# Kernel tuning notes

Measured on AMD Instinct MI355X. Metric: run time of the kernel, lower is better.

## Reference

```python
import jax, jax.numpy as jnp
import numpy as np

M = 3          # num_modes
B = 64         # batch
D = 512        # feat_dim
HIST = 5       # history_len (deque pre-filled with HIST zero matrices)
SMOOTH = 0.8   # smooth_factor


def setup_inputs() -> dict:
    ks = jax.random.split(jax.random.key(0), 6)
    return {
        "x": jax.random.normal(ks[0], (M, B, D), jnp.float32),
        "proj_W": jax.random.normal(ks[1], (M, D, D), jnp.float32) * 0.02,
        "proj_b": jnp.zeros((M, D), jnp.float32),
        "ln_g": jnp.ones((M, D), jnp.float32),
        "ln_b": jnp.zeros((M, D), jnp.float32),
        "imp_W1": jax.random.normal(ks[2], (M, D // 4, D), jnp.float32) * 0.02,
        "imp_b1": jnp.zeros((M, D // 4), jnp.float32),
        "imp_W2": jax.random.normal(ks[3], (M, D, D // 4), jnp.float32) * 0.02,
        "imp_b2": jnp.zeros((M, D), jnp.float32),
        "gamma": jax.random.normal(ks[4], (M, M), jnp.float32) * 0.1,
        "modal_bias": jax.random.normal(ks[5], (M, M), jnp.float32) * 0.01,
        "constraint": jnp.ones((M,), jnp.float32) * 0.2,
    }


def _layernorm(v, g, b, eps=1e-5):
    mu = v.mean(-1, keepdims=True)
    var = ((v - mu) ** 2).mean(-1, keepdims=True)
    return (v - mu) / jnp.sqrt(var + eps) * g + b


def reference(x, proj_W, proj_b, ln_g, ln_b, imp_W1, imp_b1, imp_W2, imp_b2,
              gamma, modal_bias, constraint):
    scale = D ** 0.5
    # per-mode projector: Linear -> LayerNorm -> ReLU
    proj = [jax.nn.relu(_layernorm(x[i] @ proj_W[i].T + proj_b[i], ln_g[i], ln_b[i]))
            for i in range(M)]
    # channel importance: Linear -> ReLU -> Linear -> Sigmoid
    cw = [jax.nn.sigmoid(
              jax.nn.relu(proj[i] @ imp_W1[i].T + imp_b1[i]) @ imp_W2[i].T + imp_b2[i])
          for i in range(M)]
    wf = [proj[i] * cw[i] for i in range(M)]  # weighted features [B, D]

    interactions, scores = [], []
    for i in range(M):
        # deque holds HIST zero matrices; appends within this forward replace
        # zeros, so the running mean is sum(appended)/HIST.
        hist_sum = jnp.zeros((D, D), x.dtype)
        hist = hist_sum / HIST
        c = constraint[i]
        feats, gs = [], []
        for j in range(M):
            if i == j:
                continue
            cur = jnp.einsum('bd,be->bde', wf[i], wf[j]) / scale  # [B, D, D]
            constrained = hist + jnp.clip(cur - hist, -c, c)
            final = SMOOTH * constrained + (1.0 - SMOOTH) * cur
            # append detached batch-mean to history
            hist_sum = hist_sum + jax.lax.stop_gradient(final.mean(0))
            hist = hist_sum / HIST
            attn = jax.nn.softmax(final, axis=-1) + modal_bias[i, j]
            g = jax.nn.sigmoid(gamma[i, j])
            attended = jnp.einsum('bde,be->bd', attn, wf[j])  # bmm(attn, value)
            feats.append(g * attended + wf[i])
            gs.append(g)
        interactions.append(jnp.stack(feats).mean(0))
        scores.append(jnp.stack(gs).mean())
    fused = jnp.stack(interactions).mean(0)              # [B, D]
    attention_weights = jax.nn.softmax(jnp.stack(scores))  # [M]
    return fused, attention_weights
```

## Files before the change

kernel.cpp:

```cpp
#include <hip/hip_runtime.h>
#include <math.h>

#define M_ 3
#define B_ 64
#define D_ 512
#define H4 128
#define HIST_ 5
#define BD (B_ * D_)
#define INVSCALE 0.04419417382415922f
#define LOG2E 1.4426950408889634f

__device__ __forceinline__ float wave_sum64(float v) {
#pragma unroll
    for (int o = 32; o >= 1; o >>= 1) v += __shfl_xor(v, o, 64);
    return v;
}

__device__ __forceinline__ float sigmoidf(float x) {
    return 1.0f / (1.0f + __expf(-x));
}

__global__ __launch_bounds__(256) void k_proj(
    const float* __restrict__ x, const float* __restrict__ pW,
    const float* __restrict__ gamma, float* __restrict__ ypart,
    float* __restrict__ out)
{
    const int m    = blockIdx.x >> 8;
    const int r    = blockIdx.x & 255;
    const int kq   = r >> 6;
    const int rem2 = r & 63;
    const int dh   = rem2 >> 5;
    const int bp   = rem2 & 31;
    const int b0   = bp << 1;
    const int t    = threadIdx.x;
    const int d    = (dh << 8) + t;

    if (blockIdx.x < 128)
        out[(blockIdx.x << 8) + t] = 0.f;

    __shared__ __align__(16) float4 xs[2][32];
    if (t < 64) {
        const int rr = t >> 5, cc = t & 31;
        xs[rr][cc] = ((const float4*)(x + (size_t)(m * B_ + b0 + rr) * D_ + kq * 128))[cc];
    }
    __syncthreads();

    const float4* wr = (const float4*)(pW + (size_t)m * D_ * D_ + (size_t)d * D_ + kq * 128);
    float acc0 = 0.f, acc1 = 0.f;
#pragma unroll
    for (int k = 0; k < 32; ++k) {
        const float4 w = wr[k];
        const float4 a = xs[0][k];
        const float4 b = xs[1][k];
        acc0 = fmaf(w.x, a.x, acc0); acc0 = fmaf(w.y, a.y, acc0);
        acc0 = fmaf(w.z, a.z, acc0); acc0 = fmaf(w.w, a.w, acc0);
        acc1 = fmaf(w.x, b.x, acc1); acc1 = fmaf(w.y, b.y, acc1);
        acc1 = fmaf(w.z, b.z, acc1); acc1 = fmaf(w.w, b.w, acc1);
    }
    const size_t idx0 = (size_t)(m * B_ + b0) * 2048 + kq * 512 + d;
    ypart[idx0]        = acc0;
    ypart[idx0 + 2048] = acc1;

    if (blockIdx.x == 0 && t == 0) {
        const float g01 = sigmoidf(gamma[1]), g02 = sigmoidf(gamma[2]);
        const float g10 = sigmoidf(gamma[3]), g12 = sigmoidf(gamma[5]);
        const float g20 = sigmoidf(gamma[6]), g21 = sigmoidf(gamma[7]);
        const float s0 = 0.5f * (g01 + g02);
        const float s1 = 0.5f * (g10 + g12);
        const float s2 = 0.5f * (g20 + g21);
        const float mx = fmaxf(s0, fmaxf(s1, s2));
        const float e0 = __expf(s0 - mx), e1 = __expf(s1 - mx), e2 = __expf(s2 - mx);
        const float den = e0 + e1 + e2;
        out[BD + 0] = e0 / den;
        out[BD + 1] = e1 / den;
        out[BD + 2] = e2 / den;
    }
}

__global__ __launch_bounds__(512) void k_lnmlp(
    const float* __restrict__ ypart, const float* __restrict__ pb,
    const float* __restrict__ lg, const float* __restrict__ lb,
    const float* __restrict__ W1, const float* __restrict__ b1,
    const float* __restrict__ W2, const float* __restrict__ b2,
    float* __restrict__ wf, float* __restrict__ Ssum,
    float* __restrict__ out)
{
    const int m = blockIdx.x >> 6;
    const int b = blockIdx.x & 63;
    const int t = threadIdx.x;
    __shared__ __align__(16) float ps[D_];
    __shared__ __align__(16) float hs[H4];
    __shared__ __align__(16) float hpart[512];
    __shared__ float red[8];

    const size_t rbase = (size_t)(m * B_ + b) * 2048;
    const float y = ypart[rbase + t] + ypart[rbase + 512 + t]
                  + ypart[rbase + 1024 + t] + ypart[rbase + 1536 + t]
                  + pb[m * D_ + t];

    float s = wave_sum64(y);
    if ((t & 63) == 0) red[t >> 6] = s;
    __syncthreads();
    const float mean = (red[0]+red[1]+red[2]+red[3]+red[4]+red[5]+red[6]+red[7]) * (1.f / D_);
    __syncthreads();
    const float v = y - mean;
    float vs = wave_sum64(v * v);
    if ((t & 63) == 0) red[t >> 6] = vs;
    __syncthreads();
    const float inv = rsqrtf((red[0]+red[1]+red[2]+red[3]+red[4]+red[5]+red[6]+red[7]) * (1.f / D_) + 1e-5f);
    const float p = fmaxf(fmaf(v * inv, lg[m * D_ + t], lb[m * D_ + t]), 0.f);
    ps[t] = p;
    __syncthreads();

    {
        const int r = t & 127, seg = t >> 7;
        const float4* w1 = (const float4*)(W1 + ((size_t)m * H4 + r) * D_) + (seg << 5);
        const float4* pv = (const float4*)ps + (seg << 5);
        float a1 = 0.f;
#pragma unroll
        for (int k = 0; k < 32; ++k) {
            const float4 w = w1[k], pp = pv[k];
            a1 = fmaf(w.x, pp.x, a1); a1 = fmaf(w.y, pp.y, a1);
            a1 = fmaf(w.z, pp.z, a1); a1 = fmaf(w.w, pp.w, a1);
        }
        hpart[t] = a1;
    }
    __syncthreads();
    if (t < H4)
        hs[t] = fmaxf(hpart[t] + hpart[t + 128] + hpart[t + 256] + hpart[t + 384]
                      + b1[m * H4 + t], 0.f);
    __syncthreads();

    const float4* w2 = (const float4*)(W2 + ((size_t)m * D_ + t) * H4);
    const float4* hv = (const float4*)hs;
    float a2 = 0.f;
#pragma unroll
    for (int k = 0; k < H4 / 4; ++k) {
        const float4 w = w2[k], hh = hv[k];
        a2 = fmaf(w.x, hh.x, a2); a2 = fmaf(w.y, hh.y, a2);
        a2 = fmaf(w.z, hh.z, a2); a2 = fmaf(w.w, hh.w, a2);
    }
    const float cw = sigmoidf(a2 + b2[m * D_ + t]);
    const float wv = p * cw;
    wf[(size_t)(m * B_ + b) * D_ + t] = wv;
    atomicAdd(&out[b * D_ + t], wv * (1.f / 3.f));

    float tot = wave_sum64(wv);
    if ((t & 63) == 0) red[t >> 6] = tot;
    __syncthreads();
    if (t == 0)
        Ssum[m * B_ + b] = red[0]+red[1]+red[2]+red[3]+red[4]+red[5]+red[6]+red[7];
}

__global__ __launch_bounds__(256) void k_fuseAH(
    const float* __restrict__ wf, const float* __restrict__ constraint,
    const float* __restrict__ gamma, const float* __restrict__ mbias,
    const float* __restrict__ Ssum, float* __restrict__ HT,
    float* __restrict__ out)
{
    const int t = threadIdx.x;

    if (blockIdx.x < 768) {
        const int i    = blockIdx.x >> 8;
        const int rem  = blockIdx.x & 255;
        const int b0   = (rem >> 4) << 2;
        const int dc   = rem & 15;
        const int ln   = t & 31;
        const int d    = (dc << 5) + ln;
        const int esec = t >> 5;
        const int jA   = (i == 0) ? 1 : 0;

        const float c08 = constraint[i] * (0.8f * LOG2E);
        float a08[4], a02[4];
        const float* uAp[4];
#pragma unroll
        for (int bb = 0; bb < 4; ++bb) {
            const float a = wf[(size_t)i * BD + (b0 + bb) * D_ + d];
            a08[bb] = a * (0.8f * INVSCALE * LOG2E);
            a02[bb] = a * (0.2f * INVSCALE * LOG2E);
            uAp[bb] = wf + (size_t)jA * BD + (b0 + bb) * D_ + (esec << 6);
        }

        float sA[4] = {0.f, 0.f, 0.f, 0.f};
        float dA[4] = {0.f, 0.f, 0.f, 0.f};
#pragma unroll 2
        for (int e = 0; e < 64; e += 4) {
#pragma unroll
            for (int bb = 0; bb < 4; ++bb) {
                const float4 u4 = *(const float4*)(uAp[bb] + e);
                const float uu[4] = {u4.x, u4.y, u4.z, u4.w};
#pragma unroll
                for (int k = 0; k < 4; ++k) {
                    const float v1 = a08[bb] * uu[k];
                    const float v2 = fminf(v1, c08);
                    const float f  = fmaf(a02[bb], uu[k], v2);
                    const float p  = __builtin_amdgcn_exp2f(f);
                    sA[bb] += p;
                    dA[bb] = fmaf(p, uu[k], dA[bb]);
                }
            }
        }

        __shared__ __align__(8) float2 part[4][256];
#pragma unroll
        for (int bb = 0; bb < 4; ++bb)
            part[bb][t] = make_float2(sA[bb], dA[bb]);
        __syncthreads();
        if (t < 128) {
            const int bb = t >> 5;
            const int l  = t & 31;
            float Ss = 0.f, Sd = 0.f;
#pragma unroll
            for (int k = 0; k < 8; ++k) {
                const float2 pp = part[bb][l + (k << 5)];
                Ss += pp.x; Sd += pp.y;
            }
            const float gA = sigmoidf(gamma[i * 3 + jA]);
            const float pv = gA * (Sd / Ss + mbias[i * 3 + jA] * Ssum[jA * B_ + b0 + bb]);
            atomicAdd(&out[(b0 + bb) * D_ + (dc << 5) + l], pv * (1.f / 6.f));
        }
        return;
    }

    const int hb = blockIdx.x - 768;
    const int i  = hb >> 7;
    const int e0 = (hb & 127) << 2;
    const int j  = (i == 0) ? 1 : 0;
    const float c = constraint[i];
    const float* wfi = wf + (size_t)i * BD;
    const float* wfj = wf + (size_t)j * BD;

    float h0[4] = {0.f, 0.f, 0.f, 0.f};
    float h1[4] = {0.f, 0.f, 0.f, 0.f};
#pragma unroll 2
    for (int b = 0; b < B_; ++b) {
        const float a0 = wfi[b * D_ + t]       * INVSCALE;
        const float a1 = wfi[b * D_ + t + 256] * INVSCALE;
        const float4 u4 = *(const float4*)(wfj + b * D_ + e0);
        const float uu[4] = {u4.x, u4.y, u4.z, u4.w};
#pragma unroll
        for (int k = 0; k < 4; ++k) {
            float tt = a0 * uu[k]; float mm = fminf(tt, c);
            h0[k] = fmaf(0.8f, mm, fmaf(0.2f, tt, h0[k]));
            tt = a1 * uu[k]; mm = fminf(tt, c);
            h1[k] = fmaf(0.8f, mm, fmaf(0.2f, tt, h1[k]));
        }
    }
    const float hsc = LOG2E / (float)(B_ * HIST_);
    float* r0 = HT + ((size_t)(i << 9) + e0) * D_;
#pragma unroll
    for (int k = 0; k < 4; ++k) {
        r0[(size_t)k * D_ + t]       = h0[k] * hsc;
        r0[(size_t)k * D_ + t + 256] = h1[k] * hsc;
    }
}

__global__ __launch_bounds__(256) void k_passB(
    const float* __restrict__ wf, const float* __restrict__ constraint,
    const float* __restrict__ gamma, const float* __restrict__ mbias,
    const float* __restrict__ HT, const float* __restrict__ Ssum,
    float* __restrict__ out)
{
    const int i    = blockIdx.x >> 8;
    const int rem  = blockIdx.x & 255;
    const int b0   = (rem >> 4) << 2;
    const int dc   = rem & 15;
    const int t    = threadIdx.x;
    const int ln   = t & 31;
    const int d    = (dc << 5) + ln;
    const int esec = t >> 5;
    const int jB   = (i == 2) ? 1 : 2;

    const float cl = constraint[i] * LOG2E;
    float a[4];
    const float* uBp[4];
#pragma unroll
    for (int bb = 0; bb < 4; ++bb) {
        a[bb]  = wf[(size_t)i * BD + (b0 + bb) * D_ + d] * (INVSCALE * LOG2E);
        uBp[bb] = wf + (size_t)jB * BD + (b0 + bb) * D_ + (esec << 6);
    }
    const float* hp = HT + ((size_t)(i << 9) + (esec << 6)) * D_ + d;

    float sB[4] = {0.f, 0.f, 0.f, 0.f};
    float dB[4] = {0.f, 0.f, 0.f, 0.f};
#pragma unroll 2
    for (int e = 0; e < 64; e += 4) {
        float hh[4];
#pragma unroll
        for (int k = 0; k < 4; ++k) hh[k] = hp[(size_t)(e + k) * D_];
#pragma unroll
        for (int bb = 0; bb < 4; ++bb) {
            const float4 u4 = *(const float4*)(uBp[bb] + e);
            const float uu[4] = {u4.x, u4.y, u4.z, u4.w};
#pragma unroll
            for (int k = 0; k < 4; ++k) {
                const float tt = a[bb] * uu[k];
                const float df = tt - hh[k];
                const float mm = fminf(fmaxf(df, -cl), cl);
                const float f  = fmaf(0.8f, hh[k] + mm, 0.2f * tt);
                const float p  = __builtin_amdgcn_exp2f(f);
                sB[bb] += p;
                dB[bb] = fmaf(p, uu[k], dB[bb]);
            }
        }
    }

    __shared__ __align__(8) float2 part[4][256];
#pragma unroll
    for (int bb = 0; bb < 4; ++bb)
        part[bb][t] = make_float2(sB[bb], dB[bb]);
    __syncthreads();
    if (t < 128) {
        const int bb = t >> 5;
        const int l  = t & 31;
        float Ss = 0.f, Sd = 0.f;
#pragma unroll
        for (int k = 0; k < 8; ++k) {
            const float2 pp = part[bb][l + (k << 5)];
            Ss += pp.x; Sd += pp.y;
        }
        const float gB = sigmoidf(gamma[i * 3 + jB]);
        const float pv = gB * (Sd / Ss + mbias[i * 3 + jB] * Ssum[jB * B_ + b0 + bb]);
        atomicAdd(&out[(b0 + bb) * D_ + (dc << 5) + l], pv * (1.f / 6.f));
    }
}

extern "C" void kernel_launch(void* const* d_in, const int* in_sizes, int n_in,
                              void* d_out, int out_size, void* d_ws, size_t ws_size,
                              hipStream_t stream) {
    const float* x    = (const float*)d_in[0];
    const float* pW   = (const float*)d_in[1];
    const float* pb   = (const float*)d_in[2];
    const float* lg   = (const float*)d_in[3];
    const float* lb   = (const float*)d_in[4];
    const float* W1   = (const float*)d_in[5];
    const float* b1   = (const float*)d_in[6];
    const float* W2   = (const float*)d_in[7];
    const float* b2   = (const float*)d_in[8];
    const float* gamma= (const float*)d_in[9];
    const float* mb   = (const float*)d_in[10];
    const float* cons = (const float*)d_in[11];
    float* out = (float*)d_out;

    float* ws    = (float*)d_ws;
    float* wf    = ws;
    float* Ssum  = ws + 98304;
    float* HT    = ws + 98496;
    float* ypart = ws + 884928;

    k_proj  <<<dim3(768),     dim3(256), 0, stream>>>(x, pW, gamma, ypart, out);
    k_lnmlp <<<dim3(M_ * B_), dim3(512), 0, stream>>>(ypart, pb, lg, lb, W1, b1, W2, b2, wf, Ssum, out);
    k_fuseAH<<<dim3(1152),    dim3(256), 0, stream>>>(wf, cons, gamma, mb, Ssum, HT, out);
    k_passB <<<dim3(768),     dim3(256), 0, stream>>>(wf, cons, gamma, mb, HT, Ssum, out);
}
```

Baseline: 153.5 us.

## Fuse four kernel launches into one cooperative persistent kernel with grid syncs

Replaces the four separate launches (projection, layernorm+MLP, pass A with history, pass B) with a single cooperative kernel of 512 blocks that loops over the work items and separates the stages with grid.sync(). It keeps the old multi-launch path as a fallback if the cooperative launch fails. The aim is to remove launch gaps and inter-kernel overhead between the stages. In exchange, the grid is capped at 512 blocks, so stages with 768 or 1152 work items run in multiple rounds. The layernorm stage now runs on only 192 blocks of 256 threads, where it previously used 512 threads per block, and grid barriers add their own cost.

```diff
diff --git a/kernel.cpp b/kernel.cpp
--- a/kernel.cpp
+++ b/kernel.cpp
@@ -1,5 +1,8 @@
 #include <hip/hip_runtime.h>
+#include <hip/hip_cooperative_groups.h>
 #include <math.h>
+
+namespace cg = cooperative_groups;
 
 #define M_ 3
 #define B_ 64
@@ -9,6 +12,7 @@
 #define BD (B_ * D_)
 #define INVSCALE 0.04419417382415922f
 #define LOG2E 1.4426950408889634f
+#define GRID 512
 
 __device__ __forceinline__ float wave_sum64(float v) {
 #pragma unroll
@@ -18,6 +22,317 @@
 
 __device__ __forceinline__ float sigmoidf(float x) {
     return 1.0f / (1.0f + __expf(-x));
+}
+
+__global__ __launch_bounds__(256, 2) void k_fused(
+    const float* __restrict__ x, const float* __restrict__ pW,
+    const float* __restrict__ pb, const float* __restrict__ lg,
+    const float* __restrict__ lb, const float* __restrict__ W1,
+    const float* __restrict__ b1, const float* __restrict__ W2,
+    const float* __restrict__ b2, const float* __restrict__ gamma,
+    const float* __restrict__ mbias, const float* __restrict__ cons,
+    float* __restrict__ wf, float* __restrict__ Ssum,
+    float* __restrict__ HT, float* __restrict__ ypart,
+    float* __restrict__ out)
+{
+    cg::grid_group grid = cg::this_grid();
+    const int t   = threadIdx.x;
+    const int bid = blockIdx.x;
+    __shared__ __align__(16) float smem[2176];
+
+    if (bid < 128)
+        out[(bid << 8) + t] = 0.f;
+
+    for (int w = bid; w < 768; w += GRID) {
+        const int m    = w >> 8;
+        const int r    = w & 255;
+        const int kq   = r >> 6;
+        const int rem2 = r & 63;
+        const int dh   = rem2 >> 5;
+        const int b0   = (rem2 & 31) << 1;
+        const int d    = (dh << 8) + t;
+
+        float4* xs = (float4*)smem;
+        if (t < 64)
+            xs[t] = ((const float4*)(x + (size_t)(m * B_ + b0 + (t >> 5)) * D_ + kq * 128))[t & 31];
+        __syncthreads();
+
+        const float4* wr = (const float4*)(pW + (size_t)m * D_ * D_ + (size_t)d * D_ + kq * 128);
+        float acc0 = 0.f, acc1 = 0.f;
+#pragma unroll
+        for (int k = 0; k < 32; ++k) {
+            const float4 wv4 = wr[k];
+            const float4 a = xs[k];
+            const float4 b = xs[32 + k];
+            acc0 = fmaf(wv4.x, a.x, acc0); acc0 = fmaf(wv4.y, a.y, acc0);
+            acc0 = fmaf(wv4.z, a.z, acc0); acc0 = fmaf(wv4.w, a.w, acc0);
+            acc1 = fmaf(wv4.x, b.x, acc1); acc1 = fmaf(wv4.y, b.y, acc1);
+            acc1 = fmaf(wv4.z, b.z, acc1); acc1 = fmaf(wv4.w, b.w, acc1);
+        }
+        const size_t idx0 = (size_t)(m * B_ + b0) * 2048 + kq * 512 + d;
+        ypart[idx0]        = acc0;
+        ypart[idx0 + 2048] = acc1;
+        __syncthreads();
+    }
+
+    if (bid == 0 && t == 0) {
+        const float g01 = sigmoidf(gamma[1]), g02 = sigmoidf(gamma[2]);
+        const float g10 = sigmoidf(gamma[3]), g12 = sigmoidf(gamma[5]);
+        const float g20 = sigmoidf(gamma[6]), g21 = sigmoidf(gamma[7]);
+        const float s0 = 0.5f * (g01 + g02);
+        const float s1 = 0.5f * (g10 + g12);
+        const float s2 = 0.5f * (g20 + g21);
+        const float mx = fmaxf(s0, fmaxf(s1, s2));
+        const float e0 = __expf(s0 - mx), e1 = __expf(s1 - mx), e2 = __expf(s2 - mx);
+        const float den = e0 + e1 + e2;
+        out[BD + 0] = e0 / den;
+        out[BD + 1] = e1 / den;
+        out[BD + 2] = e2 / den;
+    }
+
+    grid.sync();
+
+    if (bid < 192) {
+        const int m = bid >> 6;
+        const int b = bid & 63;
+        float* ps    = smem;
+        float* hpart = smem + 512;
+        float* hs    = smem + 768;
+        float* red   = smem + 896;
+
+        const size_t rbase = (size_t)(m * B_ + b) * 2048;
+        const float y0 = ypart[rbase + t]        + ypart[rbase + 512 + t]
+                       + ypart[rbase + 1024 + t] + ypart[rbase + 1536 + t]
+                       + pb[m * D_ + t];
+        const float y1 = ypart[rbase + t + 256]        + ypart[rbase + 512 + t + 256]
+                       + ypart[rbase + 1024 + t + 256] + ypart[rbase + 1536 + t + 256]
+                       + pb[m * D_ + t + 256];
+
+        float s = wave_sum64(y0 + y1);
+        if ((t & 63) == 0) red[t >> 6] = s;
+        __syncthreads();
+        const float mean = (red[0] + red[1] + red[2] + red[3]) * (1.f / D_);
+        __syncthreads();
+        const float v0 = y0 - mean, v1 = y1 - mean;
+        float vs = wave_sum64(v0 * v0 + v1 * v1);
+        if ((t & 63) == 0) red[t >> 6] = vs;
+        __syncthreads();
+        const float inv = rsqrtf((red[0] + red[1] + red[2] + red[3]) * (1.f / D_) + 1e-5f);
+        const float p0 = fmaxf(fmaf(v0 * inv, lg[m * D_ + t],       lb[m * D_ + t]),       0.f);
+        const float p1 = fmaxf(fmaf(v1 * inv, lg[m * D_ + t + 256], lb[m * D_ + t + 256]), 0.f);
+        ps[t]       = p0;
+        ps[t + 256] = p1;
+        __syncthreads();
+
+        {
+            const int r = t & 127, seg = t >> 7;
+            const float4* w1 = (const float4*)(W1 + ((size_t)m * H4 + r) * D_) + (seg << 6);
+            const float4* pv = (const float4*)ps + (seg << 6);
+            float a1 = 0.f;
+#pragma unroll
+            for (int k = 0; k < 64; ++k) {
+                const float4 wq = w1[k], pp = pv[k];
+                a1 = fmaf(wq.x, pp.x, a1); a1 = fmaf(wq.y, pp.y, a1);
+                a1 = fmaf(wq.z, pp.z, a1); a1 = fmaf(wq.w, pp.w, a1);
+            }
+            hpart[t] = a1;
+        }
+        __syncthreads();
+        if (t < H4)
+            hs[t] = fmaxf(hpart[t] + hpart[t + 128] + b1[m * H4 + t], 0.f);
+        __syncthreads();
+
+        const float4* w2a = (const float4*)(W2 + ((size_t)m * D_ + t) * H4);
+        const float4* w2b = (const float4*)(W2 + ((size_t)m * D_ + t + 256) * H4);
+        const float4* hv  = (const float4*)hs;
+        float a2_0 = 0.f, a2_1 = 0.f;
+#pragma unroll
+        for (int k = 0; k < H4 / 4; ++k) {
+            const float4 hh4 = hv[k];
+            const float4 wA = w2a[k], wB = w2b[k];
+            a2_0 = fmaf(wA.x, hh4.x, a2_0); a2_0 = fmaf(wA.y, hh4.y, a2_0);
+            a2_0 = fmaf(wA.z, hh4.z, a2_0); a2_0 = fmaf(wA.w, hh4.w, a2_0);
+            a2_1 = fmaf(wB.x, hh4.x, a2_1); a2_1 = fmaf(wB.y, hh4.y, a2_1);
+            a2_1 = fmaf(wB.z, hh4.z, a2_1); a2_1 = fmaf(wB.w, hh4.w, a2_1);
+        }
+        const float wv0 = p0 * sigmoidf(a2_0 + b2[m * D_ + t]);
+        const float wv1 = p1 * sigmoidf(a2_1 + b2[m * D_ + t + 256]);
+        wf[(size_t)(m * B_ + b) * D_ + t]       = wv0;
+        wf[(size_t)(m * B_ + b) * D_ + t + 256] = wv1;
+        atomicAdd(&out[b * D_ + t],       wv0 * (1.f / 3.f));
+        atomicAdd(&out[b * D_ + t + 256], wv1 * (1.f / 3.f));
+
+        float tot = wave_sum64(wv0 + wv1);
+        if ((t & 63) == 0) red[t >> 6] = tot;
+        __syncthreads();
+        if (t == 0)
+            Ssum[m * B_ + b] = red[0] + red[1] + red[2] + red[3];
+    }
+
+    grid.sync();
+
+    for (int w = bid; w < 1152; w += GRID) {
+        if (w < 768) {
+            const int i    = w >> 8;
+            const int rem  = w & 255;
+            const int b0   = (rem >> 4) << 2;
+            const int dc   = rem & 15;
+            const int ln   = t & 31;
+            const int d    = (dc << 5) + ln;
+            const int esec = t >> 5;
+            const int jA   = (i == 0) ? 1 : 0;
+
+            const float c08 = cons[i] * (0.8f * LOG2E);
+            float a08[4], a02[4];
+            const float* uAp[4];
+#pragma unroll
+            for (int bb = 0; bb < 4; ++bb) {
+                const float a = wf[(size_t)i * BD + (b0 + bb) * D_ + d];
+                a08[bb] = a * (0.8f * INVSCALE * LOG2E);
+                a02[bb] = a * (0.2f * INVSCALE * LOG2E);
+                uAp[bb] = wf + (size_t)jA * BD + (b0 + bb) * D_ + (esec << 6);
+            }
+
+            float sA[4] = {0.f, 0.f, 0.f, 0.f};
+            float dA[4] = {0.f, 0.f, 0.f, 0.f};
+#pragma unroll 2
+            for (int e = 0; e < 64; e += 4) {
+#pragma unroll
+                for (int bb = 0; bb < 4; ++bb) {
+                    const float4 u4 = *(const float4*)(uAp[bb] + e);
+                    const float uu[4] = {u4.x, u4.y, u4.z, u4.w};
+#pragma unroll
+                    for (int k = 0; k < 4; ++k) {
+                        const float v1 = a08[bb] * uu[k];
+                        const float v2 = fminf(v1, c08);
+                        const float f  = fmaf(a02[bb], uu[k], v2);
+                        const float p  = __builtin_amdgcn_exp2f(f);
+                        sA[bb] += p;
+                        dA[bb] = fmaf(p, uu[k], dA[bb]);
+                    }
+                }
+            }
+
+            float2* part = (float2*)smem;
+#pragma unroll
+            for (int bb = 0; bb < 4; ++bb)
+                part[bb * 256 + t] = make_float2(sA[bb], dA[bb]);
+            __syncthreads();
+            if (t < 128) {
+                const int bb = t >> 5;
+                const int l  = t & 31;
+                float Ss = 0.f, Sd = 0.f;
+#pragma unroll
+                for (int k = 0; k < 8; ++k) {
+                    const float2 pp = part[bb * 256 + l + (k << 5)];
+                    Ss += pp.x; Sd += pp.y;
+                }
+                const float gA = sigmoidf(gamma[i * 3 + jA]);
+                const float pv = gA * (Sd / Ss + mbias[i * 3 + jA] * Ssum[jA * B_ + b0 + bb]);
+                atomicAdd(&out[(b0 + bb) * D_ + (dc << 5) + l], pv * (1.f / 6.f));
+            }
+            __syncthreads();
+        } else {
+            const int hw = w - 768;
+            const int i  = hw >> 7;
+            const int e0 = (hw & 127) << 2;
+            const int j  = (i == 0) ? 1 : 0;
+            const float c = cons[i];
+            const float* wfi = wf + (size_t)i * BD;
+            const float* wfj = wf + (size_t)j * BD;
+
+            float h0[4] = {0.f, 0.f, 0.f, 0.f};
+            float h1[4] = {0.f, 0.f, 0.f, 0.f};
+#pragma unroll 2
+            for (int b = 0; b < B_; ++b) {
+                const float a0 = wfi[b * D_ + t]       * INVSCALE;
+                const float a1 = wfi[b * D_ + t + 256] * INVSCALE;
+                const float4 u4 = *(const float4*)(wfj + b * D_ + e0);
+                const float uu[4] = {u4.x, u4.y, u4.z, u4.w};
+#pragma unroll
+                for (int k = 0; k < 4; ++k) {
+                    float tt = a0 * uu[k]; float mm = fminf(tt, c);
+                    h0[k] = fmaf(0.8f, mm, fmaf(0.2f, tt, h0[k]));
+                    tt = a1 * uu[k]; mm = fminf(tt, c);
+                    h1[k] = fmaf(0.8f, mm, fmaf(0.2f, tt, h1[k]));
+                }
+            }
+            const float hsc = LOG2E / (float)(B_ * HIST_);
+            float* r0 = HT + ((size_t)(i << 9) + e0) * D_;
+#pragma unroll
+            for (int k = 0; k < 4; ++k) {
+                r0[(size_t)k * D_ + t]       = h0[k] * hsc;
+                r0[(size_t)k * D_ + t + 256] = h1[k] * hsc;
+            }
+        }
+    }
+
+    grid.sync();
+
+    for (int w = bid; w < 768; w += GRID) {
+        const int i    = w >> 8;
+        const int rem  = w & 255;
+        const int b0   = (rem >> 4) << 2;
+        const int dc   = rem & 15;
+        const int ln   = t & 31;
+        const int d    = (dc << 5) + ln;
+        const int esec = t >> 5;
+        const int jB   = (i == 2) ? 1 : 2;
+
+        const float cl = cons[i] * LOG2E;
+        float a[4];
+        const float* uBp[4];
+#pragma unroll
+        for (int bb = 0; bb < 4; ++bb) {
+            a[bb]   = wf[(size_t)i * BD + (b0 + bb) * D_ + d] * (INVSCALE * LOG2E);
+            uBp[bb] = wf + (size_t)jB * BD + (b0 + bb) * D_ + (esec << 6);
+        }
+        const float* hp = HT + ((size_t)(i << 9) + (esec << 6)) * D_ + d;
+
+        float sB[4] = {0.f, 0.f, 0.f, 0.f};
+        float dB[4] = {0.f, 0.f, 0.f, 0.f};
+#pragma unroll 2
+        for (int e = 0; e < 64; e += 4) {
+            float hh[4];
+#pragma unroll
+            for (int k = 0; k < 4; ++k) hh[k] = hp[(size_t)(e + k) * D_];
+#pragma unroll
+            for (int bb = 0; bb < 4; ++bb) {
+                const float4 u4 = *(const float4*)(uBp[bb] + e);
+                const float uu[4] = {u4.x, u4.y, u4.z, u4.w};
+#pragma unroll
+                for (int k = 0; k < 4; ++k) {
+                    const float tt = a[bb] * uu[k];
+                    const float df = tt - hh[k];
+                    const float mm = fminf(fmaxf(df, -cl), cl);
+                    const float f  = fmaf(0.8f, hh[k] + mm, 0.2f * tt);
+                    const float p  = __builtin_amdgcn_exp2f(f);
+                    sB[bb] += p;
+                    dB[bb] = fmaf(p, uu[k], dB[bb]);
+                }
+            }
+        }
+
+        float2* part = (float2*)smem;
+#pragma unroll
+        for (int bb = 0; bb < 4; ++bb)
+            part[bb * 256 + t] = make_float2(sB[bb], dB[bb]);
+        __syncthreads();
+        if (t < 128) {
+            const int bb = t >> 5;
+            const int l  = t & 31;
+            float Ss = 0.f, Sd = 0.f;
+#pragma unroll
+            for (int k = 0; k < 8; ++k) {
+                const float2 pp = part[bb * 256 + l + (k << 5)];
+                Ss += pp.x; Sd += pp.y;
+            }
+            const float gB = sigmoidf(gamma[i * 3 + jB]);
+            const float pv = gB * (Sd / Ss + mbias[i * 3 + jB] * Ssum[jB * B_ + b0 + bb]);
+            atomicAdd(&out[(b0 + bb) * D_ + (dc << 5) + l], pv * (1.f / 6.f));
+        }
+        __syncthreads();
+    }
 }
 
 __global__ __launch_bounds__(256) void k_proj(
@@ -348,8 +663,17 @@
     float* HT    = ws + 98496;
     float* ypart = ws + 884928;
 
-    k_proj  <<<dim3(768),     dim3(256), 0, stream>>>(x, pW, gamma, ypart, out);
-    k_lnmlp <<<dim3(M_ * B_), dim3(512), 0, stream>>>(ypart, pb, lg, lb, W1, b1, W2, b2, wf, Ssum, out);
-    k_fuseAH<<<dim3(1152),    dim3(256), 0, stream>>>(wf, cons, gamma, mb, Ssum, HT, out);
-    k_passB <<<dim3(768),     dim3(256), 0, stream>>>(wf, cons, gamma, mb, HT, Ssum, out);
-}
+    void* args[] = { (void*)&x, (void*)&pW, (void*)&pb, (void*)&lg, (void*)&lb,
+                     (void*)&W1, (void*)&b1, (void*)&W2, (void*)&b2, (void*)&gamma,
+                     (void*)&mb, (void*)&cons, (void*)&wf, (void*)&Ssum,
+                     (void*)&HT, (void*)&ypart, (void*)&out };
+    hipError_t err = hipLaunchCooperativeKernel(
+        reinterpret_cast<const void*>(k_fused), dim3(GRID), dim3(256),
+        (void**)args, 0, stream);
+    if (err != hipSuccess) {
+        k_proj  <<<dim3(768),     dim3(256), 0, stream>>>(x, pW, gamma, ypart, out);
+        k_lnmlp <<<dim3(M_ * B_), dim3(512), 0, stream>>>(ypart, pb, lg, lb, W1, b1, W2, b2, wf, Ssum, out);
+        k_fuseAH<<<dim3(1152),    dim3(256), 0, stream>>>(wf, cons, gamma, mb, Ssum, HT, out);
+        k_passB <<<dim3(768),     dim3(256), 0, stream>>>(wf, cons, gamma, mb, HT, Ssum, out);
+    }
+}
```

After: 368.2 us. 2.4x slower.

## Fuse projection with LN/MLP and merge both attention passes into one kernel

Applied to the files above, without the earlier changes.

The projection GEMV now runs inside the LayerNorm/MLP kernel with one block per (mode,batch) row, so the ypart partial buffer and its kernel launch are gone. The history kernel is split out on its own, and the pass-A and pass-B attention kernels are merged into one kernel that loops over all three modes for 2 batch rows per block. That kernel writes the output directly, with no atomics and no zero-init. The cost is less parallelism: the projection now uses 192 blocks each reading a full 512x512 weight slice, and the merged pass uses 512 blocks.

```diff
diff --git a/kernel.cpp b/kernel.cpp
--- a/kernel.cpp
+++ b/kernel.cpp
@@ -20,46 +20,95 @@
     return 1.0f / (1.0f + __expf(-x));
 }
 
-__global__ __launch_bounds__(256) void k_proj(
+__global__ __launch_bounds__(512) void k_projln(
     const float* __restrict__ x, const float* __restrict__ pW,
-    const float* __restrict__ gamma, float* __restrict__ ypart,
+    const float* __restrict__ pb, const float* __restrict__ lg,
+    const float* __restrict__ lb, const float* __restrict__ W1,
+    const float* __restrict__ b1, const float* __restrict__ W2,
+    const float* __restrict__ b2, const float* __restrict__ gamma,
+    float* __restrict__ wf, float* __restrict__ Ssum,
     float* __restrict__ out)
 {
-    const int m    = blockIdx.x >> 8;
-    const int r    = blockIdx.x & 255;
-    const int kq   = r >> 6;
-    const int rem2 = r & 63;
-    const int dh   = rem2 >> 5;
-    const int bp   = rem2 & 31;
-    const int b0   = bp << 1;
-    const int t    = threadIdx.x;
-    const int d    = (dh << 8) + t;
-
-    if (blockIdx.x < 128)
-        out[(blockIdx.x << 8) + t] = 0.f;
-
-    __shared__ __align__(16) float4 xs[2][32];
-    if (t < 64) {
-        const int rr = t >> 5, cc = t & 31;
-        xs[rr][cc] = ((const float4*)(x + (size_t)(m * B_ + b0 + rr) * D_ + kq * 128))[cc];
-    }
-    __syncthreads();
-
-    const float4* wr = (const float4*)(pW + (size_t)m * D_ * D_ + (size_t)d * D_ + kq * 128);
-    float acc0 = 0.f, acc1 = 0.f;
-#pragma unroll
-    for (int k = 0; k < 32; ++k) {
-        const float4 w = wr[k];
-        const float4 a = xs[0][k];
-        const float4 b = xs[1][k];
-        acc0 = fmaf(w.x, a.x, acc0); acc0 = fmaf(w.y, a.y, acc0);
-        acc0 = fmaf(w.z, a.z, acc0); acc0 = fmaf(w.w, a.w, acc0);
-        acc1 = fmaf(w.x, b.x, acc1); acc1 = fmaf(w.y, b.y, acc1);
-        acc1 = fmaf(w.z, b.z, acc1); acc1 = fmaf(w.w, b.w, acc1);
-    }
-    const size_t idx0 = (size_t)(m * B_ + b0) * 2048 + kq * 512 + d;
-    ypart[idx0]        = acc0;
-    ypart[idx0 + 2048] = acc1;
+    const int m = blockIdx.x >> 6;
+    const int b = blockIdx.x & 63;
+    const int t = threadIdx.x;
+    __shared__ __align__(16) float xs[D_];
+    __shared__ __align__(16) float ps[D_];
+    __shared__ __align__(16) float hpart[512];
+    __shared__ __align__(16) float hs[H4];
+    __shared__ float red[8];
+
+    xs[t] = x[(size_t)(m * B_ + b) * D_ + t];
+    __syncthreads();
+
+    const float4* wr = (const float4*)(pW + ((size_t)m * D_ + t) * D_);
+    const float4* xv = (const float4*)xs;
+    float q[4];
+#pragma unroll
+    for (int qq = 0; qq < 4; ++qq) {
+        float acc = 0.f;
+#pragma unroll
+        for (int k = 0; k < 32; ++k) {
+            const float4 w = wr[(qq << 5) + k];
+            const float4 a = xv[(qq << 5) + k];
+            acc = fmaf(w.x, a.x, acc); acc = fmaf(w.y, a.y, acc);
+            acc = fmaf(w.z, a.z, acc); acc = fmaf(w.w, a.w, acc);
+        }
+        q[qq] = acc;
+    }
+    const float y = q[0] + q[1] + q[2] + q[3] + pb[m * D_ + t];
+
+    float s = wave_sum64(y);
+    if ((t & 63) == 0) red[t >> 6] = s;
+    __syncthreads();
+    const float mean = (red[0]+red[1]+red[2]+red[3]+red[4]+red[5]+red[6]+red[7]) * (1.f / D_);
+    __syncthreads();
+    const float v = y - mean;
+    float vs = wave_sum64(v * v);
+    if ((t & 63) == 0) red[t >> 6] = vs;
+    __syncthreads();
+    const float inv = rsqrtf((red[0]+red[1]+red[2]+red[3]+red[4]+red[5]+red[6]+red[7]) * (1.f / D_) + 1e-5f);
+    const float p = fmaxf(fmaf(v * inv, lg[m * D_ + t], lb[m * D_ + t]), 0.f);
+    ps[t] = p;
+    __syncthreads();
+
+    {
+        const int r = t & 127, seg = t >> 7;
+        const float4* w1 = (const float4*)(W1 + ((size_t)m * H4 + r) * D_) + (seg << 5);
+        const float4* pv = (const float4*)ps + (seg << 5);
+        float a1 = 0.f;
+#pragma unroll
+        for (int k = 0; k < 32; ++k) {
+            const float4 w = w1[k], pp = pv[k];
+            a1 = fmaf(w.x, pp.x, a1); a1 = fmaf(w.y, pp.y, a1);
+            a1 = fmaf(w.z, pp.z, a1); a1 = fmaf(w.w, pp.w, a1);
+        }
+        hpart[t] = a1;
+    }
+    __syncthreads();
+    if (t < H4)
+        hs[t] = fmaxf(hpart[t] + hpart[t + 128] + hpart[t + 256] + hpart[t + 384]
+                      + b1[m * H4 + t], 0.f);
+    __syncthreads();
+
+    const float4* w2 = (const float4*)(W2 + ((size_t)m * D_ + t) * H4);
+    const float4* hv = (const float4*)hs;
+    float a2 = 0.f;
+#pragma unroll
+    for (int k = 0; k < H4 / 4; ++k) {
+        const float4 w = w2[k], hh = hv[k];
+        a2 = fmaf(w.x, hh.x, a2); a2 = fmaf(w.y, hh.y, a2);
+        a2 = fmaf(w.z, hh.z, a2); a2 = fmaf(w.w, hh.w, a2);
+    }
+    const float cw = sigmoidf(a2 + b2[m * D_ + t]);
+    const float wv = p * cw;
+    wf[(size_t)(m * B_ + b) * D_ + t] = wv;
+
+    float tot = wave_sum64(wv);
+    if ((t & 63) == 0) red[t >> 6] = tot;
+    __syncthreads();
+    if (t == 0)
+        Ssum[m * B_ + b] = red[0]+red[1]+red[2]+red[3]+red[4]+red[5]+red[6]+red[7];
 
     if (blockIdx.x == 0 && t == 0) {
         const float g01 = sigmoidf(gamma[1]), g02 = sigmoidf(gamma[2]);
@@ -77,156 +126,15 @@
     }
 }
 
-__global__ __launch_bounds__(512) void k_lnmlp(
-    const float* __restrict__ ypart, const float* __restrict__ pb,
-    const float* __restrict__ lg, const float* __restrict__ lb,
-    const float* __restrict__ W1, const float* __restrict__ b1,
-    const float* __restrict__ W2, const float* __restrict__ b2,
-    float* __restrict__ wf, float* __restrict__ Ssum,
-    float* __restrict__ out)
+__global__ __launch_bounds__(256) void k_hist(
+    const float* __restrict__ wf, const float* __restrict__ cons,
+    float* __restrict__ HT)
 {
-    const int m = blockIdx.x >> 6;
-    const int b = blockIdx.x & 63;
-    const int t = threadIdx.x;
-    __shared__ __align__(16) float ps[D_];
-    __shared__ __align__(16) float hs[H4];
-    __shared__ __align__(16) float hpart[512];
-    __shared__ float red[8];
-
-    const size_t rbase = (size_t)(m * B_ + b) * 2048;
-    const float y = ypart[rbase + t] + ypart[rbase + 512 + t]
-                  + ypart[rbase + 1024 + t] + ypart[rbase + 1536 + t]
-                  + pb[m * D_ + t];
-
-    float s = wave_sum64(y);
-    if ((t & 63) == 0) red[t >> 6] = s;
-    __syncthreads();
-    const float mean = (red[0]+red[1]+red[2]+red[3]+red[4]+red[5]+red[6]+red[7]) * (1.f / D_);
-    __syncthreads();
-    const float v = y - mean;
-    float vs = wave_sum64(v * v);
-    if ((t & 63) == 0) red[t >> 6] = vs;
-    __syncthreads();
-    const float inv = rsqrtf((red[0]+red[1]+red[2]+red[3]+red[4]+red[5]+red[6]+red[7]) * (1.f / D_) + 1e-5f);
-    const float p = fmaxf(fmaf(v * inv, lg[m * D_ + t], lb[m * D_ + t]), 0.f);
-    ps[t] = p;
-    __syncthreads();
-
-    {
-        const int r = t & 127, seg = t >> 7;
-        const float4* w1 = (const float4*)(W1 + ((size_t)m * H4 + r) * D_) + (seg << 5);
-        const float4* pv = (const float4*)ps + (seg << 5);
-        float a1 = 0.f;
-#pragma unroll
-        for (int k = 0; k < 32; ++k) {
-            const float4 w = w1[k], pp = pv[k];
-            a1 = fmaf(w.x, pp.x, a1); a1 = fmaf(w.y, pp.y, a1);
-            a1 = fmaf(w.z, pp.z, a1); a1 = fmaf(w.w, pp.w, a1);
-        }
-        hpart[t] = a1;
-    }
-    __syncthreads();
-    if (t < H4)
-        hs[t] = fmaxf(hpart[t] + hpart[t + 128] + hpart[t + 256] + hpart[t + 384]
-                      + b1[m * H4 + t], 0.f);
-    __syncthreads();
-
-    const float4* w2 = (const float4*)(W2 + ((size_t)m * D_ + t) * H4);
-    const float4* hv = (const float4*)hs;
-    float a2 = 0.f;
-#pragma unroll
-    for (int k = 0; k < H4 / 4; ++k) {
-        const float4 w = w2[k], hh = hv[k];
-        a2 = fmaf(w.x, hh.x, a2); a2 = fmaf(w.y, hh.y, a2);
-        a2 = fmaf(w.z, hh.z, a2); a2 = fmaf(w.w, hh.w, a2);
-    }
-    const float cw = sigmoidf(a2 + b2[m * D_ + t]);
-    const float wv = p * cw;
-    wf[(size_t)(m * B_ + b) * D_ + t] = wv;
-    atomicAdd(&out[b * D_ + t], wv * (1.f / 3.f));
-
-    float tot = wave_sum64(wv);
-    if ((t & 63) == 0) red[t >> 6] = tot;
-    __syncthreads();
-    if (t == 0)
-        Ssum[m * B_ + b] = red[0]+red[1]+red[2]+red[3]+red[4]+red[5]+red[6]+red[7];
-}
-
-__global__ __launch_bounds__(256) void k_fuseAH(
-    const float* __restrict__ wf, const float* __restrict__ constraint,
-    const float* __restrict__ gamma, const float* __restrict__ mbias,
-    const float* __restrict__ Ssum, float* __restrict__ HT,
-    float* __restrict__ out)
-{
-    const int t = threadIdx.x;
-
-    if (blockIdx.x < 768) {
-        const int i    = blockIdx.x >> 8;
-        const int rem  = blockIdx.x & 255;
-        const int b0   = (rem >> 4) << 2;
-        const int dc   = rem & 15;
-        const int ln   = t & 31;
-        const int d    = (dc << 5) + ln;
-        const int esec = t >> 5;
-        const int jA   = (i == 0) ? 1 : 0;
-
-        const float c08 = constraint[i] * (0.8f * LOG2E);
-        float a08[4], a02[4];
-        const float* uAp[4];
-#pragma unroll
-        for (int bb = 0; bb < 4; ++bb) {
-            const float a = wf[(size_t)i * BD + (b0 + bb) * D_ + d];
-            a08[bb] = a * (0.8f * INVSCALE * LOG2E);
-            a02[bb] = a * (0.2f * INVSCALE * LOG2E);
-            uAp[bb] = wf + (size_t)jA * BD + (b0 + bb) * D_ + (esec << 6);
-        }
-
-        float sA[4] = {0.f, 0.f, 0.f, 0.f};
-        float dA[4] = {0.f, 0.f, 0.f, 0.f};
-#pragma unroll 2
-        for (int e = 0; e < 64; e += 4) {
-#pragma unroll
-            for (int bb = 0; bb < 4; ++bb) {
-                const float4 u4 = *(const float4*)(uAp[bb] + e);
-                const float uu[4] = {u4.x, u4.y, u4.z, u4.w};
-#pragma unroll
-                for (int k = 0; k < 4; ++k) {
-                    const float v1 = a08[bb] * uu[k];
-                    const float v2 = fminf(v1, c08);
-                    const float f  = fmaf(a02[bb], uu[k], v2);
-                    const float p  = __builtin_amdgcn_exp2f(f);
-                    sA[bb] += p;
-                    dA[bb] = fmaf(p, uu[k], dA[bb]);
-                }
-            }
-        }
-
-        __shared__ __align__(8) float2 part[4][256];
-#pragma unroll
-        for (int bb = 0; bb < 4; ++bb)
-            part[bb][t] = make_float2(sA[bb], dA[bb]);
-        __syncthreads();
-        if (t < 128) {
-            const int bb = t >> 5;
-            const int l  = t & 31;
-            float Ss = 0.f, Sd = 0.f;
-#pragma unroll
-            for (int k = 0; k < 8; ++k) {
-                const float2 pp = part[bb][l + (k << 5)];
-                Ss += pp.x; Sd += pp.y;
-            }
-            const float gA = sigmoidf(gamma[i * 3 + jA]);
-            const float pv = gA * (Sd / Ss + mbias[i * 3 + jA] * Ssum[jA * B_ + b0 + bb]);
-            atomicAdd(&out[(b0 + bb) * D_ + (dc << 5) + l], pv * (1.f / 6.f));
-        }
-        return;
-    }
-
-    const int hb = blockIdx.x - 768;
-    const int i  = hb >> 7;
-    const int e0 = (hb & 127) << 2;
+    const int t  = threadIdx.x;
+    const int i  = blockIdx.x >> 7;
+    const int e0 = (blockIdx.x & 127) << 2;
     const int j  = (i == 0) ? 1 : 0;
-    const float c = constraint[i];
+    const float c = cons[i];
     const float* wfi = wf + (size_t)i * BD;
     const float* wfj = wf + (size_t)j * BD;
 
@@ -255,73 +163,104 @@
     }
 }
 
-__global__ __launch_bounds__(256) void k_passB(
-    const float* __restrict__ wf, const float* __restrict__ constraint,
+__global__ __launch_bounds__(256) void k_pass(
+    const float* __restrict__ wf, const float* __restrict__ cons,
     const float* __restrict__ gamma, const float* __restrict__ mbias,
     const float* __restrict__ HT, const float* __restrict__ Ssum,
     float* __restrict__ out)
 {
-    const int i    = blockIdx.x >> 8;
-    const int rem  = blockIdx.x & 255;
-    const int b0   = (rem >> 4) << 2;
-    const int dc   = rem & 15;
+    const int bg   = blockIdx.x >> 4;
+    const int dc   = blockIdx.x & 15;
+    const int b0   = bg << 1;
     const int t    = threadIdx.x;
     const int ln   = t & 31;
     const int d    = (dc << 5) + ln;
     const int esec = t >> 5;
-    const int jB   = (i == 2) ? 1 : 2;
-
-    const float cl = constraint[i] * LOG2E;
-    float a[4];
-    const float* uBp[4];
-#pragma unroll
-    for (int bb = 0; bb < 4; ++bb) {
-        a[bb]  = wf[(size_t)i * BD + (b0 + bb) * D_ + d] * (INVSCALE * LOG2E);
-        uBp[bb] = wf + (size_t)jB * BD + (b0 + bb) * D_ + (esec << 6);
-    }
-    const float* hp = HT + ((size_t)(i << 9) + (esec << 6)) * D_ + d;
-
-    float sB[4] = {0.f, 0.f, 0.f, 0.f};
-    float dB[4] = {0.f, 0.f, 0.f, 0.f};
+
+    __shared__ __align__(16) float4 part[2][256];
+    float oacc = 0.f;
+
+#pragma unroll
+    for (int i = 0; i < 3; ++i) {
+        const int jA = (i == 0) ? 1 : 0;
+        const int jB = (i == 2) ? 1 : 2;
+        const float c08 = cons[i] * (0.8f * LOG2E);
+        const float cl  = cons[i] * LOG2E;
+
+        float a08[2], a02[2], aB[2];
+        const float* uA[2];
+        const float* uB[2];
+#pragma unroll
+        for (int bb = 0; bb < 2; ++bb) {
+            const float a = wf[(size_t)i * BD + (b0 + bb) * D_ + d];
+            a08[bb] = a * (0.8f * INVSCALE * LOG2E);
+            a02[bb] = a * (0.2f * INVSCALE * LOG2E);
+            aB[bb]  = a * (INVSCALE * LOG2E);
+            uA[bb] = wf + (size_t)jA * BD + (b0 + bb) * D_ + (esec << 6);
+            uB[bb] = wf + (size_t)jB * BD + (b0 + bb) * D_ + (esec << 6);
+        }
+        const float* hp = HT + ((size_t)(i << 9) + (esec << 6)) * D_ + d;
+
+        float sA[2] = {0.f, 0.f}, dA[2] = {0.f, 0.f};
+        float sB[2] = {0.f, 0.f}, dB[2] = {0.f, 0.f};
 #pragma unroll 2
-    for (int e = 0; e < 64; e += 4) {
-        float hh[4];
-#pragma unroll
-        for (int k = 0; k < 4; ++k) hh[k] = hp[(size_t)(e + k) * D_];
-#pragma unroll
-        for (int bb = 0; bb < 4; ++bb) {
-            const float4 u4 = *(const float4*)(uBp[bb] + e);
-            const float uu[4] = {u4.x, u4.y, u4.z, u4.w};
-#pragma unroll
-            for (int k = 0; k < 4; ++k) {
-                const float tt = a[bb] * uu[k];
-                const float df = tt - hh[k];
-                const float mm = fminf(fmaxf(df, -cl), cl);
-                const float f  = fmaf(0.8f, hh[k] + mm, 0.2f * tt);
-                const float p  = __builtin_amdgcn_exp2f(f);
-                sB[bb] += p;
-                dB[bb] = fmaf(p, uu[k], dB[bb]);
+        for (int e = 0; e < 64; e += 4) {
+            float hh[4];
+#pragma unroll
+            for (int k = 0; k < 4; ++k) hh[k] = hp[(size_t)(e + k) * D_];
+#pragma unroll
+            for (int bb = 0; bb < 2; ++bb) {
+                const float4 uA4 = *(const float4*)(uA[bb] + e);
+                const float4 uB4 = *(const float4*)(uB[bb] + e);
+                const float ua[4] = {uA4.x, uA4.y, uA4.z, uA4.w};
+                const float ub[4] = {uB4.x, uB4.y, uB4.z, uB4.w};
+#pragma unroll
+                for (int k = 0; k < 4; ++k) {
+                    const float v1 = a08[bb] * ua[k];
+                    const float v2 = fminf(v1, c08);
+                    const float fA = fmaf(a02[bb], ua[k], v2);
+                    const float pA = __builtin_amdgcn_exp2f(fA);
+                    sA[bb] += pA;
+                    dA[bb] = fmaf(pA, ua[k], dA[bb]);
+                    const float tt = aB[bb] * ub[k];
+                    const float df = tt - hh[k];
+                    const float mm = fminf(fmaxf(df, -cl), cl);
+                    const float fB = fmaf(0.8f, hh[k] + mm, 0.2f * tt);
+                    const float pB = __builtin_amdgcn_exp2f(fB);
+                    sB[bb] += pB;
+                    dB[bb] = fmaf(pB, ub[k], dB[bb]);
+                }
             }
         }
-    }
-
-    __shared__ __align__(8) float2 part[4][256];
-#pragma unroll
-    for (int bb = 0; bb < 4; ++bb)
-        part[bb][t] = make_float2(sB[bb], dB[bb]);
-    __syncthreads();
-    if (t < 128) {
+
+        part[0][t] = make_float4(sA[0], dA[0], sB[0], dB[0]);
+        part[1][t] = make_float4(sA[1], dA[1], sB[1], dB[1]);
+        __syncthreads();
+        if (t < 64) {
+            const int bb = t >> 5;
+            const int l  = t & 31;
+            float SsA = 0.f, SdA = 0.f, SsB = 0.f, SdB = 0.f;
+#pragma unroll
+            for (int k = 0; k < 8; ++k) {
+                const float4 pp = part[bb][l + (k << 5)];
+                SsA += pp.x; SdA += pp.y; SsB += pp.z; SdB += pp.w;
+            }
+            const float gA = sigmoidf(gamma[i * 3 + jA]);
+            const float gB = sigmoidf(gamma[i * 3 + jB]);
+            oacc += gA * (SdA / SsA + mbias[i * 3 + jA] * Ssum[jA * B_ + b0 + bb]);
+            oacc += gB * (SdB / SsB + mbias[i * 3 + jB] * Ssum[jB * B_ + b0 + bb]);
+        }
+        __syncthreads();
+    }
+
+    if (t < 64) {
         const int bb = t >> 5;
         const int l  = t & 31;
-        float Ss = 0.f, Sd = 0.f;
-#pragma unroll
-        for (int k = 0; k < 8; ++k) {
-            const float2 pp = part[bb][l + (k << 5)];
-            Ss += pp.x; Sd += pp.y;
-        }
-        const float gB = sigmoidf(gamma[i * 3 + jB]);
-        const float pv = gB * (Sd / Ss + mbias[i * 3 + jB] * Ssum[jB * B_ + b0 + bb]);
-        atomicAdd(&out[(b0 + bb) * D_ + (dc << 5) + l], pv * (1.f / 6.f));
+        const int od = (dc << 5) + l;
+        const float w0 = wf[(size_t)0 * BD + (b0 + bb) * D_ + od];
+        const float w1 = wf[(size_t)1 * BD + (b0 + bb) * D_ + od];
+        const float w2 = wf[(size_t)2 * BD + (b0 + bb) * D_ + od];
+        out[(b0 + bb) * D_ + od] = oacc * (1.f / 6.f) + (w0 + w1 + w2) * (1.f / 3.f);
     }
 }
 
@@ -342,14 +281,12 @@
     const float* cons = (const float*)d_in[11];
     float* out = (float*)d_out;
 
-    float* ws    = (float*)d_ws;
-    float* wf    = ws;
-    float* Ssum  = ws + 98304;
-    float* HT    = ws + 98496;
-    float* ypart = ws + 884928;
-
-    k_proj  <<<dim3(768),     dim3(256), 0, stream>>>(x, pW, gamma, ypart, out);
-    k_lnmlp <<<dim3(M_ * B_), dim3(512), 0, stream>>>(ypart, pb, lg, lb, W1, b1, W2, b2, wf, Ssum, out);
-    k_fuseAH<<<dim3(1152),    dim3(256), 0, stream>>>(wf, cons, gamma, mb, Ssum, HT, out);
-    k_passB <<<dim3(768),     dim3(256), 0, stream>>>(wf, cons, gamma, mb, HT, Ssum, out);
-}
+    float* ws   = (float*)d_ws;
+    float* wf   = ws;
+    float* Ssum = ws + 98304;
+    float* HT   = ws + 98496;
+
+    k_projln<<<dim3(M_ * B_), dim3(512), 0, stream>>>(x, pW, pb, lg, lb, W1, b1, W2, b2, gamma, wf, Ssum, out);
+    k_hist  <<<dim3(384),     dim3(256), 0, stream>>>(wf, cons, HT);
+    k_pass  <<<dim3(512),     dim3(256), 0, stream>>>(wf, cons, gamma, mb, HT, Ssum, out);
+}
```

Measured after the change: 180.3 us. 1.17x slower.
